# Kernel tuning notes

Measured on AMD Instinct MI355X. Metric: run time of the kernel, lower is better.

## Reference

```python
import jax, jax.numpy as jnp
import numpy as np

S = 16384   # num src nodes
D = 16384   # num dst nodes
FS = 128    # src feature len
FD = 128    # dst feature len
R = 50.0    # dist threshold (m)
L = 2005.0  # box side so avg degree ~ 32
LN_EPS = 1e-5


def setup_inputs() -> dict:
    rng = np.random.default_rng(0)
    src_pos_np = rng.uniform(0.0, L, (S, 2)).astype(np.float32)
    dst_pos_np = rng.uniform(0.0, L, (D, 2)).astype(np.float32)
    # radius-graph edge construction (data-dependent, done once outside jit)
    es, ed = [], []
    CH = 2048
    for i in range(0, S, CH):
        d = np.linalg.norm(src_pos_np[i:i + CH, None, :] - dst_pos_np[None, :, :], axis=-1)
        si, di = np.nonzero(d <= R)
        es.append((si + i).astype(np.int32))
        ed.append(di.astype(np.int32))
    edge_src_idx = jnp.asarray(np.concatenate(es))
    edge_dst_idx = jnp.asarray(np.concatenate(ed))

    key = jax.random.key(0)
    ks = jax.random.split(key, 12)
    w = lambda k, shape: (jax.random.normal(k, shape, jnp.float32) * 0.02)
    return {
        'src_node_features': jax.random.normal(ks[0], (S, FS), jnp.float32),
        'src_node_pos': jnp.asarray(src_pos_np),
        'dst_node_features': jax.random.normal(ks[1], (D, FD), jnp.float32),
        'dst_node_pos': jnp.asarray(dst_pos_np),
        'src_w': w(ks[2], (FS, FS)), 'src_b': jnp.zeros((FS,), jnp.float32),
        'dst_w': w(ks[3], (FD, FD)), 'dst_b': jnp.zeros((FD,), jnp.float32),
        'dist_w': w(ks[4], (2, FD)), 'dist_b': jnp.zeros((FD,), jnp.float32),
        'edge_w1': w(ks[5], (FS + FD + FD, FD)), 'edge_b1': jnp.zeros((FD,), jnp.float32),
        'edge_w2': w(ks[6], (FD, FD)), 'edge_b2': jnp.zeros((FD,), jnp.float32),
        'ln_g': jnp.ones((FD,), jnp.float32), 'ln_b': jnp.zeros((FD,), jnp.float32),
        'out_w': w(ks[7], (FD, FD)), 'out_b': jnp.zeros((FD,), jnp.float32),
        'edge_src_idx': edge_src_idx,
        'edge_dst_idx': edge_dst_idx,
    }


def reference(src_node_features, src_node_pos, dst_node_features, dst_node_pos,
              src_w, src_b, dst_w, dst_b, dist_w, dist_b,
              edge_w1, edge_b1, edge_w2, edge_b2, ln_g, ln_b, out_w, out_b,
              edge_src_idx, edge_dst_idx):
    # node encoders: Linear + ReLU
    src_enc = jax.nn.relu(src_node_features @ src_w + src_b)   # [S, FS]
    dst_enc = jax.nn.relu(dst_node_features @ dst_w + dst_b)   # [D, FD]
    # gather per-edge
    e_src = src_enc[edge_src_idx]                               # [E, FS]
    e_dst = dst_enc[edge_dst_idx]                               # [E, FD]
    e_dpos = src_node_pos[edge_src_idx] - dst_node_pos[edge_dst_idx]  # [E, 2]
    e_dist = jax.nn.relu(e_dpos @ dist_w + dist_b)              # [E, FD]
    # edge MLP: Linear-ReLU-Linear on concat [E, FS+FD+FD]
    e_in = jnp.concatenate([e_src, e_dist, e_dst], axis=-1)
    e_out = jax.nn.relu(e_in @ edge_w1 + edge_b1) @ edge_w2 + edge_b2  # [E, FD]
    # scatter-add to destination nodes
    agg = dst_enc + jax.ops.segment_sum(e_out, edge_dst_idx, num_segments=D)
    # LayerNorm + ReLU + Linear + residual + ReLU
    mu = jnp.mean(agg, axis=-1, keepdims=True)
    var = jnp.mean(jnp.square(agg - mu), axis=-1, keepdims=True)
    ln = (agg - mu) * jax.lax.rsqrt(var + LN_EPS) * ln_g + ln_b
    h = jax.nn.relu(ln) @ out_w + out_b + dst_node_features
    return jax.nn.relu(h)
```

## Files before the change

kernel.cpp:

```cpp
#include <hip/hip_runtime.h>

typedef unsigned short ushort_t;
typedef unsigned int uint_t;
typedef short bhalf8 __attribute__((ext_vector_type(8)));
typedef float f32x4 __attribute__((ext_vector_type(4)));

#define DEG_CAP 96
#define PWIN 192

__device__ __forceinline__ float b2f(ushort_t u) {
    union { uint_t i; float f; } v; v.i = ((uint_t)u) << 16; return v.f;
}
__device__ __forceinline__ float u2f(uint_t u) {
    union { uint_t i; float f; } v; v.i = u; return v.f;
}
__device__ __forceinline__ ushort_t f2b(float f) {
    union { float f; uint_t i; } v; v.f = f;
    uint_t r = v.i + 0x7fffu + ((v.i >> 16) & 1u);
    return (ushort_t)(r >> 16);
}
__device__ __forceinline__ uint_t f2u(float f) {
    union { float f; uint_t i; } v; v.f = f; return v.i;
}
__device__ __forceinline__ uint_t pack_trunc(float lo, float hi) {
    return (f2u(lo) >> 16) | (f2u(hi) & 0xffff0000u);
}
__device__ __forceinline__ uint_t addpack_trunc(uint_t a, uint_t b) {
    union { uint_t i; float f; } t0, t1, s0, s1;
    t0.i = a << 16;          s0.i = b << 16;
    t1.i = a & 0xffff0000u;  s1.i = b & 0xffff0000u;
    return pack_trunc(t0.f + s0.f, t1.f + s1.f);
}

__global__ __launch_bounds__(256) void prep_kernel(
    const float* __restrict__ wsrc, const float* __restrict__ wdst,
    const float* __restrict__ w2,   const float* __restrict__ wout,
    const float* __restrict__ w1,
    ushort_t* __restrict__ msrc, ushort_t* __restrict__ mdst,
    ushort_t* __restrict__ m2,   ushort_t* __restrict__ mout,
    ushort_t* __restrict__ m1a,  ushort_t* __restrict__ m1b,
    ushort_t* __restrict__ m1c,
    const int* __restrict__ esi, const int* __restrict__ edi, int E,
    int* __restrict__ deg, int* __restrict__ bucket,
    float* __restrict__ hsum, int countB, int zeroB, int Dn)
{
    int b = blockIdx.x, tid = threadIdx.x;
    if (b < 56) {
        const float* ins[7] = { wsrc, wdst, w2, wout, w1, w1 + 16384, w1 + 32768 };
        ushort_t* outs[7]   = { msrc, mdst, m2, mout, m1a, m1b, m1c };
        int mat = b >> 3;
        const float* in = ins[mat];
        ushort_t* out = outs[mat];
        int flat = (b & 7)*256 + tid;
        int nt = flat >> 8, rem = flat & 255;
        int ks = rem >> 6, lane = rem & 63;
        int q = lane >> 4, m = lane & 15;
        #pragma unroll
        for (int j = 0; j < 8; ++j)
            out[flat*8 + j] = f2b(in[(ks*32 + q*8 + j)*128 + nt*16 + m]);
    } else if (b < 56 + countB) {
        int i = (b - 56)*256 + tid;
        if (i < E) {
            int d = edi[i];
            int p = atomicAdd(&deg[d], 1);
            if (p < DEG_CAP) bucket[(size_t)d*DEG_CAP + p] = esi[i];
        }
    } else {
        int zb = b - 56 - countB;
        float4* h4 = (float4*)hsum;
        int total4 = Dn*32;
        for (int i = zb*256 + tid; i < total4; i += zeroB*256)
            h4[i] = make_float4(0.f, 0.f, 0.f, 0.f);
    }
}

__global__ __launch_bounds__(256) void enc2_kernel(
    const float* __restrict__ src_feat, const float* __restrict__ dst_feat,
    const ushort_t* __restrict__ msrc, const ushort_t* __restrict__ mdst,
    const ushort_t* __restrict__ m1a,  const ushort_t* __restrict__ m1c,
    const float* __restrict__ src_b,   const float* __restrict__ dst_b,
    const float* __restrict__ b1,
    ushort_t* __restrict__ Csrc, ushort_t* __restrict__ Cdst,
    ushort_t* __restrict__ dst_enc,
    const int* __restrict__ deg, int* __restrict__ P,
    int* __restrict__ tileStart, int nTiles, int Dn,
    int Sb, int Db)
{
    int tid = threadIdx.x, blk = blockIdx.x;

    if (blk == Sb + Db) {
        __shared__ int sums[256];
        int per = Dn >> 8;
        const int4* d4 = (const int4*)(deg + tid*per);
        int4 v[16]; int s = 0;
        #pragma unroll
        for (int k = 0; k < 16; ++k) {
            v[k] = d4[k];
            v[k].x = min(v[k].x, DEG_CAP); v[k].y = min(v[k].y, DEG_CAP);
            v[k].z = min(v[k].z, DEG_CAP); v[k].w = min(v[k].w, DEG_CAP);
            s += v[k].x + v[k].y + v[k].z + v[k].w;
        }
        sums[tid] = s;
        __syncthreads();
        for (int off = 1; off < 256; off <<= 1) {
            int x = (tid >= off) ? sums[tid - off] : 0;
            __syncthreads();
            sums[tid] += x;
            __syncthreads();
        }
        int run = sums[tid] - s;
        int4* n4 = (int4*)(P + tid*per);
        auto wt = [&](int start, int end, int d) {
            for (int tt = (start + 63) >> 6; tt*64 < end && tt < nTiles; ++tt)
                tileStart[tt] = d;
        };
        #pragma unroll
        for (int k = 0; k < 16; ++k) {
            int d0 = tid*per + k*4;
            int4 o; int st;
            st = run; o.x = run; run += v[k].x; wt(st, run, d0 + 0);
            st = run; o.y = run; run += v[k].y; wt(st, run, d0 + 1);
            st = run; o.z = run; run += v[k].z; wt(st, run, d0 + 2);
            st = run; o.w = run; run += v[k].w; wt(st, run, d0 + 3);
            n4[k] = o;
        }
        return;
    }

    __shared__ ushort_t A_l[64*136];
    __shared__ ushort_t E_l[64*136];
    __shared__ float b_l[128];
    __shared__ float b2_l[128];

    const float* A; const ushort_t *W1m, *W2m; const float* bias; const float* bias2;
    ushort_t *outC, *outEnc; int rowbase;
    if (blk < Sb) { A = src_feat; W1m = msrc; W2m = m1a; bias = src_b;
                    outC = Csrc; outEnc = nullptr; rowbase = blk*64; bias2 = nullptr; }
    else          { A = dst_feat; W1m = mdst; W2m = m1c; bias = dst_b;
                    outC = Cdst; outEnc = dst_enc; rowbase = (blk - Sb)*64; bias2 = b1; }

    const float4* A4 = (const float4*)A;
    for (int i = tid; i < 2048; i += 256) {
        int r = i >> 5, c = i & 31;
        float4 v = A4[(size_t)(rowbase + r)*32 + c];
        uint2 u;
        u.x = pack_trunc(v.x, v.y);
        u.y = pack_trunc(v.z, v.w);
        *(uint2*)(A_l + r*136 + c*4) = u;
    }
    if (tid < 128) { b_l[tid] = bias[tid]; b2_l[tid] = bias2 ? bias2[tid] : 0.f; }
    __syncthreads();

    int lane = tid & 63, w = tid >> 6, q = lane >> 4, m = lane & 15;
    const bhalf8* Wv1 = (const bhalf8*)W1m;
    f32x4 acc[4][2] = {};
    #pragma unroll
    for (int ks = 0; ks < 4; ++ks) {
        bhalf8 bf0 = Wv1[((2*w)*4 + ks)*64 + lane];
        bhalf8 bf1 = Wv1[((2*w+1)*4 + ks)*64 + lane];
        #pragma unroll
        for (int mt = 0; mt < 4; ++mt) {
            bhalf8 a = *(const bhalf8*)(A_l + (mt*16 + m)*136 + ks*32 + q*8);
            acc[mt][0] = __builtin_amdgcn_mfma_f32_16x16x32_bf16(a, bf0, acc[mt][0], 0, 0, 0);
            acc[mt][1] = __builtin_amdgcn_mfma_f32_16x16x32_bf16(a, bf1, acc[mt][1], 0, 0, 0);
        }
    }
    #pragma unroll
    for (int mt = 0; mt < 4; ++mt)
    #pragma unroll
    for (int nt = 0; nt < 2; ++nt)
    #pragma unroll
    for (int reg = 0; reg < 4; ++reg) {
        int col = w*32 + nt*16 + m;
        int row = mt*16 + q*4 + reg;
        E_l[row*136 + col] = f2b(fmaxf(acc[mt][nt][reg] + b_l[col], 0.f));
    }
    __syncthreads();

    if (outEnc) {
        for (int i = tid; i < 1024; i += 256) {
            int r = i >> 4, c = i & 15;
            ((uint4*)outEnc)[(size_t)(rowbase + r)*16 + c] = *(const uint4*)(E_l + r*136 + c*8);
        }
    }

    const bhalf8* Wv2 = (const bhalf8*)W2m;
    f32x4 acc2[4][2] = {};
    #pragma unroll
    for (int ks = 0; ks < 4; ++ks) {
        bhalf8 bf0 = Wv2[((2*w)*4 + ks)*64 + lane];
        bhalf8 bf1 = Wv2[((2*w+1)*4 + ks)*64 + lane];
        #pragma unroll
        for (int mt = 0; mt < 4; ++mt) {
            bhalf8 a = *(const bhalf8*)(E_l + (mt*16 + m)*136 + ks*32 + q*8);
            acc2[mt][0] = __builtin_amdgcn_mfma_f32_16x16x32_bf16(a, bf0, acc2[mt][0], 0, 0, 0);
            acc2[mt][1] = __builtin_amdgcn_mfma_f32_16x16x32_bf16(a, bf1, acc2[mt][1], 0, 0, 0);
        }
    }
    #pragma unroll
    for (int mt = 0; mt < 4; ++mt)
    #pragma unroll
    for (int nt = 0; nt < 2; ++nt)
    #pragma unroll
    for (int reg = 0; reg < 4; ++reg) {
        int col = w*32 + nt*16 + m;
        int row = mt*16 + q*4 + reg;
        A_l[row*136 + col] = f2b(acc2[mt][nt][reg] + b2_l[col]);
    }
    __syncthreads();
    for (int i = tid; i < 1024; i += 256) {
        int r = i >> 4, c = i & 15;
        ((uint4*)outC)[(size_t)(rowbase + r)*16 + c] = *(const uint4*)(A_l + r*136 + c*8);
    }
}

__global__ __launch_bounds__(256, 4) void edge_kernel(
    const ushort_t* __restrict__ Csrc, const ushort_t* __restrict__ Cdst,
    const float* __restrict__ src_pos, const float* __restrict__ dst_pos,
    const int* __restrict__ P, const int* __restrict__ tileStart,
    const int* __restrict__ bucket, int E, int Dn,
    const ushort_t* __restrict__ w1bm,
    const float* __restrict__ dist_w, const float* __restrict__ dist_b,
    float* __restrict__ hsum)
{
    __shared__ char pool[17408];
    __shared__ ushort_t G[64*136];
    __shared__ int Pw[PWIN];
    __shared__ int s_l[64], d_l[64], dofs_l[64];
    __shared__ uint_t bndmask[2];
    __shared__ float dx_l[64], dy_l[64];
    __shared__ float dw0_l[128], dw1_l[128], db_l[128];

    ushort_t* X  = (ushort_t*)pool;
    ushort_t* Hc = (ushort_t*)pool;

    int tid = threadIdx.x, blk = blockIdx.x;
    int d0 = tileStart[blk];

    if (tid < PWIN) Pw[tid] = (d0 + tid < Dn) ? P[d0 + tid] : 0x7fffffff;
    if (tid < 128) {
        dw0_l[tid] = dist_w[tid];
        dw1_l[tid] = dist_w[128 + tid];
        db_l[tid]  = dist_b[tid];
    }
    __syncthreads();

    if (tid < 64) {
        int g = blk*64 + tid;
        int s = 0, d = -1;
        float dx = 0.f, dy = 0.f;
        if (g < E) {
            int i = 0;
            while (i + 1 < PWIN && Pw[i + 1] <= g) ++i;
            int p;
            if (i == PWIN - 1) {
                int lo = d0 + PWIN - 1, hi = Dn - 1;
                while (lo < hi) {
                    int mid = (lo + hi + 1) >> 1;
                    if (P[mid] <= g) lo = mid; else hi = mid - 1;
                }
                d = lo; p = g - P[lo];
            } else {
                d = d0 + i; p = g - Pw[i];
            }
            s = bucket[(size_t)d*DEG_CAP + min(p, DEG_CAP - 1)];
            float2 sp = ((const float2*)src_pos)[s];
            float2 dp = ((const float2*)dst_pos)[d];
            dx = sp.x - dp.x; dy = sp.y - dp.y;
        }
        s_l[tid] = s; d_l[tid] = d;
        dofs_l[tid] = (d >= 0) ? d*128 : -1;
        dx_l[tid] = dx; dy_l[tid] = dy;
    }
    __syncthreads();

    if (tid < 64) {
        int d = d_l[tid];
        int dn = (tid < 63) ? d_l[tid + 1] : -2;
        bool bnd = (tid == 31) || (tid == 63) || (dn != d);
        unsigned long long mask = __ballot(bnd);
        if (tid == 0) { bndmask[0] = (uint_t)mask; bndmask[1] = (uint_t)(mask >> 32); }
    }

    const uint4* cs4 = (const uint4*)Csrc;
    const uint4* cd4 = (const uint4*)Cdst;
    #pragma unroll
    for (int k = 0; k < 4; ++k) {
        int i = tid + k*256;
        int r = i >> 4, c = i & 15;
        uint4 a = cs4[(size_t)s_l[r]*16 + c];
        uint4 b = cd4[(size_t)max(d_l[r], 0)*16 + c];
        uint4 u;
        u.x = addpack_trunc(a.x, b.x);
        u.y = addpack_trunc(a.y, b.y);
        u.z = addpack_trunc(a.z, b.z);
        u.w = addpack_trunc(a.w, b.w);
        *(uint4*)(G + r*136 + c*8) = u;
    }
    for (int i = tid; i < 4096; i += 256) {
        int r = i >> 6, j2 = (i & 63)*2;
        float dx = dx_l[r], dy = dy_l[r];
        float v0 = fmaxf(fmaf(dx, dw0_l[j2],   fmaf(dy, dw1_l[j2],   db_l[j2])),   0.f);
        float v1 = fmaxf(fmaf(dx, dw0_l[j2+1], fmaf(dy, dw1_l[j2+1], db_l[j2+1])), 0.f);
        *(uint_t*)(X + r*136 + j2) = pack_trunc(v0, v1);
    }
    __syncthreads();

    int lane = tid & 63, w = tid >> 6, q = lane >> 4, m = lane & 15;
    f32x4 acc[4][2] = {};
    const bhalf8* Wv = (const bhalf8*)w1bm;
    #pragma unroll
    for (int ks = 0; ks < 4; ++ks) {
        bhalf8 bf0 = Wv[((2*w)*4 + ks)*64 + lane];
        bhalf8 bf1 = Wv[((2*w+1)*4 + ks)*64 + lane];
        #pragma unroll
        for (int mt = 0; mt < 4; ++mt) {
            bhalf8 a = *(const bhalf8*)(X + (mt*16 + m)*136 + ks*32 + q*8);
            acc[mt][0] = __builtin_amdgcn_mfma_f32_16x16x32_bf16(a, bf0, acc[mt][0], 0, 0, 0);
            acc[mt][1] = __builtin_amdgcn_mfma_f32_16x16x32_bf16(a, bf1, acc[mt][1], 0, 0, 0);
        }
    }
    __syncthreads();

    #pragma unroll
    for (int mt = 0; mt < 4; ++mt)
    #pragma unroll
    for (int nt = 0; nt < 2; ++nt) {
        int col = w*32 + nt*16 + m;
        int row0 = mt*16 + q*4;
        uint2 u;
        u.x = pack_trunc(acc[mt][nt][0], acc[mt][nt][1]);
        u.y = pack_trunc(acc[mt][nt][2], acc[mt][nt][3]);
        *(uint2*)(Hc + col*68 + row0) = u;
    }
    __syncthreads();

    {
        int j = tid & 127, h = tid >> 7;
        uint_t mask = bndmask[h];
        const ushort_t* Hcol = Hc + j*68 + h*32;
        int rbase = h*32;
        float a = 0.f;
        #pragma unroll
        for (int k8 = 0; k8 < 8; ++k8) {
            uint2 hp = *(const uint2*)(Hcol + k8*4);
            float hv[4];
            hv[0] = u2f(hp.x << 16);
            hv[1] = u2f(hp.x & 0xffff0000u);
            hv[2] = u2f(hp.y << 16);
            hv[3] = u2f(hp.y & 0xffff0000u);
            #pragma unroll
            for (int t = 0; t < 4; ++t) {
                int r = rbase + k8*4 + t;
                float g = b2f(G[r*136 + j]);
                a += fmaxf(hv[t] + g, 0.f);
                if ((mask >> (k8*4 + t)) & 1u) {
                    int ofs = dofs_l[r];
                    if (ofs >= 0) atomicAdd(&hsum[(size_t)ofs + j], a);
                    a = 0.f;
                }
            }
        }
    }
}

__global__ __launch_bounds__(256) void aggfinal16_kernel(
    const float* __restrict__ hsum, const ushort_t* __restrict__ w2m,
    const float* __restrict__ b2, const int* __restrict__ deg,
    const ushort_t* __restrict__ dst_enc, const float* __restrict__ ln_g,
    const float* __restrict__ ln_b, const ushort_t* __restrict__ moutm,
    const float* __restrict__ out_b, const float* __restrict__ dst_feat,
    float* __restrict__ out)
{
    __shared__ ushort_t A_l[16*136];
    __shared__ ushort_t E2[16*136];
    __shared__ float ps[64], ps2[64];
    __shared__ float muv[16], invv[16];
    __shared__ float pb2[128], pg[128], plb[128], pob[128];
    __shared__ int dgl[16];

    int tid = threadIdx.x, blk = blockIdx.x;
    int lane = tid & 63, w = tid >> 6, q = lane >> 4, m = lane & 15;

    if (tid < 128) { pb2[tid] = b2[tid]; pg[tid] = ln_g[tid];
                     plb[tid] = ln_b[tid]; pob[tid] = out_b[tid]; }
    if (tid < 16) dgl[tid] = deg[blk*16 + tid];
    {
        int r = tid >> 4, c = tid & 15;
        const float4* hv4 = (const float4*)hsum;
        size_t base = (size_t)(blk*16 + r)*32 + c*2;
        float4 p0 = hv4[base], p1 = hv4[base + 1];
        uint4 u;
        u.x = pack_trunc(p0.x, p0.y);
        u.y = pack_trunc(p0.z, p0.w);
        u.z = pack_trunc(p1.x, p1.y);
        u.w = pack_trunc(p1.z, p1.w);
        *(uint4*)(A_l + r*136 + c*8) = u;
        *(uint4*)(E2 + r*136 + c*8) = ((const uint4*)dst_enc)[(size_t)(blk*16 + r)*16 + c];
    }
    __syncthreads();

    const bhalf8* Wv2 = (const bhalf8*)w2m;
    f32x4 acc[2] = {};
    #pragma unroll
    for (int ks = 0; ks < 4; ++ks) {
        bhalf8 bf0 = Wv2[((2*w)*4 + ks)*64 + lane];
        bhalf8 bf1 = Wv2[((2*w+1)*4 + ks)*64 + lane];
        bhalf8 a = *(const bhalf8*)(A_l + m*136 + ks*32 + q*8);
        acc[0] = __builtin_amdgcn_mfma_f32_16x16x32_bf16(a, bf0, acc[0], 0, 0, 0);
        acc[1] = __builtin_amdgcn_mfma_f32_16x16x32_bf16(a, bf1, acc[1], 0, 0, 0);
    }
    float y[2][4];
    #pragma unroll
    for (int nt = 0; nt < 2; ++nt)
    #pragma unroll
    for (int reg = 0; reg < 4; ++reg) {
        int col = w*32 + nt*16 + m;
        int rowl = q*4 + reg;
        y[nt][reg] = acc[nt][reg] + (float)dgl[rowl]*pb2[col] + b2f(E2[rowl*136 + col]);
    }
    float s[4], s2[4];
    #pragma unroll
    for (int reg = 0; reg < 4; ++reg) {
        s[reg]  = y[0][reg] + y[1][reg];
        s2[reg] = y[0][reg]*y[0][reg] + y[1][reg]*y[1][reg];
    }
    #pragma unroll
    for (int o = 1; o < 16; o <<= 1) {
        #pragma unroll
        for (int reg = 0; reg < 4; ++reg) {
            s[reg]  += __shfl_xor(s[reg],  o);
            s2[reg] += __shfl_xor(s2[reg], o);
        }
    }
    if (m == 0) {
        #pragma unroll
        for (int reg = 0; reg < 4; ++reg) {
            ps[(q*4 + reg)*4 + w]  = s[reg];
            ps2[(q*4 + reg)*4 + w] = s2[reg];
        }
    }
    __syncthreads();
    if (tid < 16) {
        float su = ps[tid*4] + ps[tid*4+1] + ps[tid*4+2] + ps[tid*4+3];
        float sq = ps2[tid*4] + ps2[tid*4+1] + ps2[tid*4+2] + ps2[tid*4+3];
        float mu = su / 128.f;
        float var = sq / 128.f - mu*mu;
        muv[tid] = mu;
        invv[tid] = 1.0f / sqrtf(var + 1e-5f);
    }
    __syncthreads();
    #pragma unroll
    for (int nt = 0; nt < 2; ++nt)
    #pragma unroll
    for (int reg = 0; reg < 4; ++reg) {
        int col = w*32 + nt*16 + m;
        int rowl = q*4 + reg;
        float v = (y[nt][reg] - muv[rowl])*invv[rowl]*pg[col] + plb[col];
        A_l[rowl*136 + col] = f2b(fmaxf(v, 0.f));
    }
    __syncthreads();

    const bhalf8* Wo = (const bhalf8*)moutm;
    f32x4 acc2[2] = {};
    #pragma unroll
    for (int ks = 0; ks < 4; ++ks) {
        bhalf8 bf0 = Wo[((2*w)*4 + ks)*64 + lane];
        bhalf8 bf1 = Wo[((2*w+1)*4 + ks)*64 + lane];
        bhalf8 a = *(const bhalf8*)(A_l + m*136 + ks*32 + q*8);
        acc2[0] = __builtin_amdgcn_mfma_f32_16x16x32_bf16(a, bf0, acc2[0], 0, 0, 0);
        acc2[1] = __builtin_amdgcn_mfma_f32_16x16x32_bf16(a, bf1, acc2[1], 0, 0, 0);
    }
    #pragma unroll
    for (int nt = 0; nt < 2; ++nt)
    #pragma unroll
    for (int reg = 0; reg < 4; ++reg) {
        int col = w*32 + nt*16 + m;
        size_t grow = (size_t)blk*16 + q*4 + reg;
        float v = acc2[nt][reg] + pob[col] + dst_feat[grow*128 + col];
        out[grow*128 + col] = fmaxf(v, 0.f);
    }
}

extern "C" void kernel_launch(void* const* d_in, const int* in_sizes, int n_in,
                              void* d_out, int out_size, void* d_ws, size_t ws_size,
                              hipStream_t stream)
{
    const float* src_feat = (const float*)d_in[0];
    const float* src_pos  = (const float*)d_in[1];
    const float* dst_feat = (const float*)d_in[2];
    const float* dst_pos  = (const float*)d_in[3];
    const float* src_w    = (const float*)d_in[4];
    const float* src_b    = (const float*)d_in[5];
    const float* dst_w    = (const float*)d_in[6];
    const float* dst_b    = (const float*)d_in[7];
    const float* dist_w   = (const float*)d_in[8];
    const float* dist_b   = (const float*)d_in[9];
    const float* w1       = (const float*)d_in[10];
    const float* b1       = (const float*)d_in[11];
    const float* w2       = (const float*)d_in[12];
    const float* b2       = (const float*)d_in[13];
    const float* ln_g     = (const float*)d_in[14];
    const float* ln_b     = (const float*)d_in[15];
    const float* out_w    = (const float*)d_in[16];
    const float* out_b    = (const float*)d_in[17];
    const int* esi        = (const int*)d_in[18];
    const int* edi        = (const int*)d_in[19];
    int E = in_sizes[18];
    int S = in_sizes[0] / 128;
    int D = in_sizes[2] / 128;
    int nTiles = (E + 63) / 64;

    char* ws = (char*)d_ws;
    size_t off = 0;
    auto alloc = [&](size_t bytes) { char* p = ws + off; off += (bytes + 511) & ~(size_t)511; return p; };
    ushort_t* Csrc    = (ushort_t*)alloc((size_t)S*128*2);
    ushort_t* Cdst    = (ushort_t*)alloc((size_t)D*128*2);
    ushort_t* dst_enc = (ushort_t*)alloc((size_t)D*128*2);
    float*    hsum    = (float*)   alloc((size_t)D*128*4);
    ushort_t* t_src   = (ushort_t*)alloc(128*128*2);
    ushort_t* t_dst   = (ushort_t*)alloc(128*128*2);
    ushort_t* t_w2    = (ushort_t*)alloc(128*128*2);
    ushort_t* t_out   = (ushort_t*)alloc(128*128*2);
    ushort_t* t_1a    = (ushort_t*)alloc(128*128*2);
    ushort_t* t_1b    = (ushort_t*)alloc(128*128*2);
    ushort_t* t_1c    = (ushort_t*)alloc(128*128*2);
    int*      deg     = (int*)     alloc((size_t)D*4);
    int*      P       = (int*)     alloc((size_t)D*4);
    int*      tileS   = (int*)     alloc((size_t)nTiles*4);
    int*      bucket  = (int*)     alloc((size_t)D*DEG_CAP*4);

    hipMemsetAsync(deg, 0, (size_t)D*4, stream);

    int countB = (E + 255)/256;
    int zeroB = 256;
    prep_kernel<<<56 + countB + zeroB, 256, 0, stream>>>(
        src_w, dst_w, w2, out_w, w1,
        t_src, t_dst, t_w2, t_out, t_1a, t_1b, t_1c,
        esi, edi, E, deg, bucket, hsum, countB, zeroB, D);

    int Sb = S/64, Db = D/64;
    enc2_kernel<<<Sb + Db + 1, 256, 0, stream>>>(
        src_feat, dst_feat, t_src, t_dst, t_1a, t_1c, src_b, dst_b, b1,
        Csrc, Cdst, dst_enc, deg, P, tileS, nTiles, D, Sb, Db);

    edge_kernel<<<nTiles, 256, 0, stream>>>(
        Csrc, Cdst, src_pos, dst_pos, P, tileS, bucket, E, D,
        t_1b, dist_w, dist_b, hsum);

    aggfinal16_kernel<<<D/16, 256, 0, stream>>>(
        hsum, t_w2, b2, deg, dst_enc, ln_g, ln_b,
        t_out, out_b, dst_feat, (float*)d_out);
}
```

Baseline: 210.3 us.

## Process four edge tiles per block with register-resident W1 fragments

The edge kernel now loops over four consecutive 64-edge tiles per block instead of one. The W1 MFMA weight fragments and the distance weights are loaded once per block and held in registers and shared memory. A search hint carries the destination position forward between tiles, and the P window grows to 384 entries to cover the larger span. This cuts per-block setup and weight reloads, at the cost of four times fewer blocks, which lowers parallelism and adds barriers within each block.

```diff
diff --git a/kernel.cpp b/kernel.cpp
--- a/kernel.cpp
+++ b/kernel.cpp
@@ -6,7 +6,8 @@
 typedef float f32x4 __attribute__((ext_vector_type(4)));
 
 #define DEG_CAP 96
-#define PWIN 192
+#define PWIN 384
+#define TPB_TILES 4
 
 __device__ __forceinline__ float b2f(ushort_t u) {
     union { uint_t i; float f; } v; v.i = ((uint_t)u) << 16; return v.f;
@@ -218,7 +219,7 @@
     const ushort_t* __restrict__ Csrc, const ushort_t* __restrict__ Cdst,
     const float* __restrict__ src_pos, const float* __restrict__ dst_pos,
     const int* __restrict__ P, const int* __restrict__ tileStart,
-    const int* __restrict__ bucket, int E, int Dn,
+    const int* __restrict__ bucket, int E, int Dn, int nTiles,
     const ushort_t* __restrict__ w1bm,
     const float* __restrict__ dist_w, const float* __restrict__ dist_b,
     float* __restrict__ hsum)
@@ -228,6 +229,7 @@
     __shared__ int Pw[PWIN];
     __shared__ int s_l[64], d_l[64], dofs_l[64];
     __shared__ uint_t bndmask[2];
+    __shared__ int hint_l;
     __shared__ float dx_l[64], dy_l[64];
     __shared__ float dw0_l[128], dw1_l[128], db_l[128];
 
@@ -235,129 +237,140 @@
     ushort_t* Hc = (ushort_t*)pool;
 
     int tid = threadIdx.x, blk = blockIdx.x;
-    int d0 = tileStart[blk];
-
-    if (tid < PWIN) Pw[tid] = (d0 + tid < Dn) ? P[d0 + tid] : 0x7fffffff;
+    int t0 = blk*TPB_TILES;
+    int d0 = tileStart[t0];
+
+    for (int k = tid; k < PWIN; k += 256)
+        Pw[k] = (d0 + k < Dn) ? P[d0 + k] : 0x7fffffff;
     if (tid < 128) {
         dw0_l[tid] = dist_w[tid];
         dw1_l[tid] = dist_w[128 + tid];
         db_l[tid]  = dist_b[tid];
     }
-    __syncthreads();
-
-    if (tid < 64) {
-        int g = blk*64 + tid;
-        int s = 0, d = -1;
-        float dx = 0.f, dy = 0.f;
-        if (g < E) {
-            int i = 0;
-            while (i + 1 < PWIN && Pw[i + 1] <= g) ++i;
-            int p;
-            if (i == PWIN - 1) {
-                int lo = d0 + PWIN - 1, hi = Dn - 1;
-                while (lo < hi) {
-                    int mid = (lo + hi + 1) >> 1;
-                    if (P[mid] <= g) lo = mid; else hi = mid - 1;
-                }
-                d = lo; p = g - P[lo];
-            } else {
-                d = d0 + i; p = g - Pw[i];
-            }
-            s = bucket[(size_t)d*DEG_CAP + min(p, DEG_CAP - 1)];
-            float2 sp = ((const float2*)src_pos)[s];
-            float2 dp = ((const float2*)dst_pos)[d];
-            dx = sp.x - dp.x; dy = sp.y - dp.y;
-        }
-        s_l[tid] = s; d_l[tid] = d;
-        dofs_l[tid] = (d >= 0) ? d*128 : -1;
-        dx_l[tid] = dx; dy_l[tid] = dy;
-    }
-    __syncthreads();
-
-    if (tid < 64) {
-        int d = d_l[tid];
-        int dn = (tid < 63) ? d_l[tid + 1] : -2;
-        bool bnd = (tid == 31) || (tid == 63) || (dn != d);
-        unsigned long long mask = __ballot(bnd);
-        if (tid == 0) { bndmask[0] = (uint_t)mask; bndmask[1] = (uint_t)(mask >> 32); }
-    }
-
+    if (tid == 0) hint_l = 0;
+
+    int lane = tid & 63, w = tid >> 6, q = lane >> 4, m = lane & 15;
+    const bhalf8* Wv = (const bhalf8*)w1bm;
+    bhalf8 wf0[4], wf1[4];
+    #pragma unroll
+    for (int ks = 0; ks < 4; ++ks) {
+        wf0[ks] = Wv[((2*w)*4 + ks)*64 + lane];
+        wf1[ks] = Wv[((2*w+1)*4 + ks)*64 + lane];
+    }
     const uint4* cs4 = (const uint4*)Csrc;
     const uint4* cd4 = (const uint4*)Cdst;
-    #pragma unroll
-    for (int k = 0; k < 4; ++k) {
-        int i = tid + k*256;
-        int r = i >> 4, c = i & 15;
-        uint4 a = cs4[(size_t)s_l[r]*16 + c];
-        uint4 b = cd4[(size_t)max(d_l[r], 0)*16 + c];
-        uint4 u;
-        u.x = addpack_trunc(a.x, b.x);
-        u.y = addpack_trunc(a.y, b.y);
-        u.z = addpack_trunc(a.z, b.z);
-        u.w = addpack_trunc(a.w, b.w);
-        *(uint4*)(G + r*136 + c*8) = u;
-    }
-    for (int i = tid; i < 4096; i += 256) {
-        int r = i >> 6, j2 = (i & 63)*2;
-        float dx = dx_l[r], dy = dy_l[r];
-        float v0 = fmaxf(fmaf(dx, dw0_l[j2],   fmaf(dy, dw1_l[j2],   db_l[j2])),   0.f);
-        float v1 = fmaxf(fmaf(dx, dw0_l[j2+1], fmaf(dy, dw1_l[j2+1], db_l[j2+1])), 0.f);
-        *(uint_t*)(X + r*136 + j2) = pack_trunc(v0, v1);
-    }
-    __syncthreads();
-
-    int lane = tid & 63, w = tid >> 6, q = lane >> 4, m = lane & 15;
-    f32x4 acc[4][2] = {};
-    const bhalf8* Wv = (const bhalf8*)w1bm;
-    #pragma unroll
-    for (int ks = 0; ks < 4; ++ks) {
-        bhalf8 bf0 = Wv[((2*w)*4 + ks)*64 + lane];
-        bhalf8 bf1 = Wv[((2*w+1)*4 + ks)*64 + lane];
-        #pragma unroll
-        for (int mt = 0; mt < 4; ++mt) {
-            bhalf8 a = *(const bhalf8*)(X + (mt*16 + m)*136 + ks*32 + q*8);
-            acc[mt][0] = __builtin_amdgcn_mfma_f32_16x16x32_bf16(a, bf0, acc[mt][0], 0, 0, 0);
-            acc[mt][1] = __builtin_amdgcn_mfma_f32_16x16x32_bf16(a, bf1, acc[mt][1], 0, 0, 0);
-        }
-    }
-    __syncthreads();
-
-    #pragma unroll
-    for (int mt = 0; mt < 4; ++mt)
-    #pragma unroll
-    for (int nt = 0; nt < 2; ++nt) {
-        int col = w*32 + nt*16 + m;
-        int row0 = mt*16 + q*4;
-        uint2 u;
-        u.x = pack_trunc(acc[mt][nt][0], acc[mt][nt][1]);
-        u.y = pack_trunc(acc[mt][nt][2], acc[mt][nt][3]);
-        *(uint2*)(Hc + col*68 + row0) = u;
-    }
-    __syncthreads();
-
-    {
-        int j = tid & 127, h = tid >> 7;
-        uint_t mask = bndmask[h];
-        const ushort_t* Hcol = Hc + j*68 + h*32;
-        int rbase = h*32;
-        float a = 0.f;
-        #pragma unroll
-        for (int k8 = 0; k8 < 8; ++k8) {
-            uint2 hp = *(const uint2*)(Hcol + k8*4);
-            float hv[4];
-            hv[0] = u2f(hp.x << 16);
-            hv[1] = u2f(hp.x & 0xffff0000u);
-            hv[2] = u2f(hp.y << 16);
-            hv[3] = u2f(hp.y & 0xffff0000u);
+    __syncthreads();
+
+    int tEnd = min(t0 + TPB_TILES, nTiles);
+    for (int t = t0; t < tEnd; ++t) {
+        if (t != t0) __syncthreads();
+
+        if (tid < 64) {
+            int g = t*64 + tid;
+            int s = 0, d = -1;
+            float dx = 0.f, dy = 0.f;
+            if (g < E) {
+                int i = hint_l;
+                while (i + 1 < PWIN && Pw[i + 1] <= g) ++i;
+                int p;
+                if (i == PWIN - 1) {
+                    int lo = d0 + PWIN - 1, hi = Dn - 1;
+                    while (lo < hi) {
+                        int mid = (lo + hi + 1) >> 1;
+                        if (P[mid] <= g) lo = mid; else hi = mid - 1;
+                    }
+                    d = lo; p = g - P[lo];
+                } else {
+                    d = d0 + i; p = g - Pw[i];
+                }
+                s = bucket[(size_t)d*DEG_CAP + min(p, DEG_CAP - 1)];
+                float2 sp = ((const float2*)src_pos)[s];
+                float2 dp = ((const float2*)dst_pos)[d];
+                dx = sp.x - dp.x; dy = sp.y - dp.y;
+            }
+            s_l[tid] = s; d_l[tid] = d;
+            dofs_l[tid] = (d >= 0) ? d*128 : -1;
+            dx_l[tid] = dx; dy_l[tid] = dy;
+            int dd = d_l[tid];
+            int dn = (tid < 63) ? d_l[tid + 1] : -2;
+            bool bnd = (tid == 31) || (tid == 63) || (dn != dd);
+            unsigned long long mask = __ballot(bnd);
+            if (tid == 0) { bndmask[0] = (uint_t)mask; bndmask[1] = (uint_t)(mask >> 32); }
+            if (tid == 63 && dd >= 0) hint_l = max(dd - d0, 0);
+        }
+        __syncthreads();
+
+        #pragma unroll
+        for (int k = 0; k < 4; ++k) {
+            int i = tid + k*256;
+            int r = i >> 4, c = i & 15;
+            uint4 a = cs4[(size_t)s_l[r]*16 + c];
+            uint4 b = cd4[(size_t)max(d_l[r], 0)*16 + c];
+            uint4 u;
+            u.x = addpack_trunc(a.x, b.x);
+            u.y = addpack_trunc(a.y, b.y);
+            u.z = addpack_trunc(a.z, b.z);
+            u.w = addpack_trunc(a.w, b.w);
+            *(uint4*)(G + r*136 + c*8) = u;
+        }
+        for (int i = tid; i < 4096; i += 256) {
+            int r = i >> 6, j2 = (i & 63)*2;
+            float dx = dx_l[r], dy = dy_l[r];
+            float v0 = fmaxf(fmaf(dx, dw0_l[j2],   fmaf(dy, dw1_l[j2],   db_l[j2])),   0.f);
+            float v1 = fmaxf(fmaf(dx, dw0_l[j2+1], fmaf(dy, dw1_l[j2+1], db_l[j2+1])), 0.f);
+            *(uint_t*)(X + r*136 + j2) = pack_trunc(v0, v1);
+        }
+        __syncthreads();
+
+        f32x4 acc[4][2] = {};
+        #pragma unroll
+        for (int ks = 0; ks < 4; ++ks) {
             #pragma unroll
-            for (int t = 0; t < 4; ++t) {
-                int r = rbase + k8*4 + t;
-                float g = b2f(G[r*136 + j]);
-                a += fmaxf(hv[t] + g, 0.f);
-                if ((mask >> (k8*4 + t)) & 1u) {
-                    int ofs = dofs_l[r];
-                    if (ofs >= 0) atomicAdd(&hsum[(size_t)ofs + j], a);
-                    a = 0.f;
+            for (int mt = 0; mt < 4; ++mt) {
+                bhalf8 a = *(const bhalf8*)(X + (mt*16 + m)*136 + ks*32 + q*8);
+                acc[mt][0] = __builtin_amdgcn_mfma_f32_16x16x32_bf16(a, wf0[ks], acc[mt][0], 0, 0, 0);
+                acc[mt][1] = __builtin_amdgcn_mfma_f32_16x16x32_bf16(a, wf1[ks], acc[mt][1], 0, 0, 0);
+            }
+        }
+        __syncthreads();
+
+        #pragma unroll
+        for (int mt = 0; mt < 4; ++mt)
+        #pragma unroll
+        for (int nt = 0; nt < 2; ++nt) {
+            int col = w*32 + nt*16 + m;
+            int row0 = mt*16 + q*4;
+            uint2 u;
+            u.x = pack_trunc(acc[mt][nt][0], acc[mt][nt][1]);
+            u.y = pack_trunc(acc[mt][nt][2], acc[mt][nt][3]);
+            *(uint2*)(Hc + col*68 + row0) = u;
+        }
+        __syncthreads();
+
+        {
+            int j = tid & 127, h = tid >> 7;
+            uint_t mask = bndmask[h];
+            const ushort_t* Hcol = Hc + j*68 + h*32;
+            int rbase = h*32;
+            float a = 0.f;
+            #pragma unroll
+            for (int k8 = 0; k8 < 8; ++k8) {
+                uint2 hp = *(const uint2*)(Hcol + k8*4);
+                float hv[4];
+                hv[0] = u2f(hp.x << 16);
+                hv[1] = u2f(hp.x & 0xffff0000u);
+                hv[2] = u2f(hp.y << 16);
+                hv[3] = u2f(hp.y & 0xffff0000u);
+                #pragma unroll
+                for (int tt = 0; tt < 4; ++tt) {
+                    int r = rbase + k8*4 + tt;
+                    float g = b2f(G[r*136 + j]);
+                    a += fmaxf(hv[tt] + g, 0.f);
+                    if ((mask >> (k8*4 + tt)) & 1u) {
+                        int ofs = dofs_l[r];
+                        if (ofs >= 0) atomicAdd(&hsum[(size_t)ofs + j], a);
+                        a = 0.f;
+                    }
                 }
             }
         }
@@ -544,8 +557,9 @@
         src_feat, dst_feat, t_src, t_dst, t_1a, t_1c, src_b, dst_b, b1,
         Csrc, Cdst, dst_enc, deg, P, tileS, nTiles, D, Sb, Db);
 
-    edge_kernel<<<nTiles, 256, 0, stream>>>(
-        Csrc, Cdst, src_pos, dst_pos, P, tileS, bucket, E, D,
+    int nBlocks = (nTiles + TPB_TILES - 1) / TPB_TILES;
+    edge_kernel<<<nBlocks, 256, 0, stream>>>(
+        Csrc, Cdst, src_pos, dst_pos, P, tileS, bucket, E, D, nTiles,
         t_1b, dist_w, dist_b, hsum);
 
     aggfinal16_kernel<<<D/16, 256, 0, stream>>>(
```

After: 210.6 us. No clear change (+0.1%).

## Run edge kernel with 512 threads, one 16-column MFMA slice per wave

Applied to the files above, without the earlier changes.

Doubles the edge kernel block to 512 threads (8 waves). Each wave now computes one 16-column N-tile of the first-layer MFMA instead of two, and the segmented reduction splits rows into 16-row quarters with boundary flags every 16 rows. The index setup and boundary ballot are merged so one barrier is removed. The aim is more waves to hide gather and MFMA latency, at the cost of more atomics from the finer segments and higher occupancy pressure.

```diff
diff --git a/kernel.cpp b/kernel.cpp
--- a/kernel.cpp
+++ b/kernel.cpp
@@ -214,7 +214,7 @@
     }
 }
 
-__global__ __launch_bounds__(256, 4) void edge_kernel(
+__global__ __launch_bounds__(512, 8) void edge_kernel(
     const ushort_t* __restrict__ Csrc, const ushort_t* __restrict__ Cdst,
     const float* __restrict__ src_pos, const float* __restrict__ dst_pos,
     const int* __restrict__ P, const int* __restrict__ tileStart,
@@ -271,22 +271,19 @@
         s_l[tid] = s; d_l[tid] = d;
         dofs_l[tid] = (d >= 0) ? d*128 : -1;
         dx_l[tid] = dx; dy_l[tid] = dy;
-    }
-    __syncthreads();
-
-    if (tid < 64) {
-        int d = d_l[tid];
+        int dd = d_l[tid];
         int dn = (tid < 63) ? d_l[tid + 1] : -2;
-        bool bnd = (tid == 31) || (tid == 63) || (dn != d);
+        bool bnd = ((tid & 15) == 15) || (dn != dd);
         unsigned long long mask = __ballot(bnd);
         if (tid == 0) { bndmask[0] = (uint_t)mask; bndmask[1] = (uint_t)(mask >> 32); }
     }
+    __syncthreads();
 
     const uint4* cs4 = (const uint4*)Csrc;
     const uint4* cd4 = (const uint4*)Cdst;
     #pragma unroll
-    for (int k = 0; k < 4; ++k) {
-        int i = tid + k*256;
+    for (int k = 0; k < 2; ++k) {
+        int i = tid + k*512;
         int r = i >> 4, c = i & 15;
         uint4 a = cs4[(size_t)s_l[r]*16 + c];
         uint4 b = cd4[(size_t)max(d_l[r], 0)*16 + c];
@@ -297,7 +294,7 @@
         u.w = addpack_trunc(a.w, b.w);
         *(uint4*)(G + r*136 + c*8) = u;
     }
-    for (int i = tid; i < 4096; i += 256) {
+    for (int i = tid; i < 4096; i += 512) {
         int r = i >> 6, j2 = (i & 63)*2;
         float dx = dx_l[r], dy = dy_l[r];
         float v0 = fmaxf(fmaf(dx, dw0_l[j2],   fmaf(dy, dw1_l[j2],   db_l[j2])),   0.f);
@@ -307,43 +304,39 @@
     __syncthreads();
 
     int lane = tid & 63, w = tid >> 6, q = lane >> 4, m = lane & 15;
-    f32x4 acc[4][2] = {};
+    f32x4 acc[4] = {};
     const bhalf8* Wv = (const bhalf8*)w1bm;
     #pragma unroll
     for (int ks = 0; ks < 4; ++ks) {
-        bhalf8 bf0 = Wv[((2*w)*4 + ks)*64 + lane];
-        bhalf8 bf1 = Wv[((2*w+1)*4 + ks)*64 + lane];
+        bhalf8 bf = Wv[(w*4 + ks)*64 + lane];
         #pragma unroll
         for (int mt = 0; mt < 4; ++mt) {
             bhalf8 a = *(const bhalf8*)(X + (mt*16 + m)*136 + ks*32 + q*8);
-            acc[mt][0] = __builtin_amdgcn_mfma_f32_16x16x32_bf16(a, bf0, acc[mt][0], 0, 0, 0);
-            acc[mt][1] = __builtin_amdgcn_mfma_f32_16x16x32_bf16(a, bf1, acc[mt][1], 0, 0, 0);
-        }
-    }
-    __syncthreads();
-
-    #pragma unroll
-    for (int mt = 0; mt < 4; ++mt)
-    #pragma unroll
-    for (int nt = 0; nt < 2; ++nt) {
-        int col = w*32 + nt*16 + m;
+            acc[mt] = __builtin_amdgcn_mfma_f32_16x16x32_bf16(a, bf, acc[mt], 0, 0, 0);
+        }
+    }
+    __syncthreads();
+
+    #pragma unroll
+    for (int mt = 0; mt < 4; ++mt) {
+        int col = w*16 + m;
         int row0 = mt*16 + q*4;
         uint2 u;
-        u.x = pack_trunc(acc[mt][nt][0], acc[mt][nt][1]);
-        u.y = pack_trunc(acc[mt][nt][2], acc[mt][nt][3]);
+        u.x = pack_trunc(acc[mt][0], acc[mt][1]);
+        u.y = pack_trunc(acc[mt][2], acc[mt][3]);
         *(uint2*)(Hc + col*68 + row0) = u;
     }
     __syncthreads();
 
     {
         int j = tid & 127, h = tid >> 7;
-        uint_t mask = bndmask[h];
-        const ushort_t* Hcol = Hc + j*68 + h*32;
-        int rbase = h*32;
+        uint_t mask = bndmask[h >> 1] >> ((h & 1)*16);
+        const ushort_t* Hcol = Hc + j*68 + h*16;
+        int rbase = h*16;
         float a = 0.f;
         #pragma unroll
-        for (int k8 = 0; k8 < 8; ++k8) {
-            uint2 hp = *(const uint2*)(Hcol + k8*4);
+        for (int k4 = 0; k4 < 4; ++k4) {
+            uint2 hp = *(const uint2*)(Hcol + k4*4);
             float hv[4];
             hv[0] = u2f(hp.x << 16);
             hv[1] = u2f(hp.x & 0xffff0000u);
@@ -351,10 +344,10 @@
             hv[3] = u2f(hp.y & 0xffff0000u);
             #pragma unroll
             for (int t = 0; t < 4; ++t) {
-                int r = rbase + k8*4 + t;
+                int r = rbase + k4*4 + t;
                 float g = b2f(G[r*136 + j]);
                 a += fmaxf(hv[t] + g, 0.f);
-                if ((mask >> (k8*4 + t)) & 1u) {
+                if ((mask >> (k4*4 + t)) & 1u) {
                     int ofs = dofs_l[r];
                     if (ofs >= 0) atomicAdd(&hsum[(size_t)ofs + j], a);
                     a = 0.f;
@@ -544,7 +537,7 @@
         src_feat, dst_feat, t_src, t_dst, t_1a, t_1c, src_b, dst_b, b1,
         Csrc, Cdst, dst_enc, deg, P, tileS, nTiles, D, Sb, Db);
 
-    edge_kernel<<<nTiles, 256, 0, stream>>>(
+    edge_kernel<<<nTiles, 512, 0, stream>>>(
         Csrc, Cdst, src_pos, dst_pos, P, tileS, bucket, E, D,
         t_1b, dist_w, dist_b, hsum);
 
```

Measured after the change: 208.1 us. About the same (-1.1%).
